# Performance work log

Hardware: AMD Instinct MI355X
Metric: run time of the kernel (lower is better)

The kernel has to match this reference:

```python
import jax, jax.numpy as jnp
import numpy as np

N_L = 1600   # sample_number_l
N_R = 64     # sample_number_r
F = 512      # num_rgbxyz_feature


def setup_inputs() -> dict:
    key = jax.random.key(0)
    ks = jax.random.split(key, 6)
    soutput_l = jax.random.normal(ks[0], (200000, F), dtype=jnp.float32)
    soutput_r = jax.random.normal(ks[1], (100000, F), dtype=jnp.float32)
    W1 = jax.random.normal(ks[2], (2 * F, 512), dtype=jnp.float32) * 0.02
    b1 = jnp.zeros((512,), dtype=jnp.float32)
    W2 = jax.random.normal(ks[3], (512, 2), dtype=jnp.float32) * 0.02
    b2 = jnp.zeros((2,), dtype=jnp.float32)
    sample_idx_l = jax.random.randint(ks[4], (N_L,), 0, 200000)
    sample_idx_r = jax.random.randint(ks[5], (N_R,), 0, 100000)
    return {
        'soutput_l': soutput_l, 'soutput_r': soutput_r,
        'W1': W1, 'b1': b1, 'W2': W2, 'b2': b2,
        'sample_idx_l': sample_idx_l, 'sample_idx_r': sample_idx_r,
    }


def reference(soutput_l, soutput_r, W1, b1, W2, b2, sample_idx_l, sample_idx_r):
    # Gather sampled per-point features (replaces torch.randint sampling)
    fl = soutput_l[sample_idx_l]          # [N_l, F]
    fr = soutput_r[sample_idx_r]          # [N_r, F]
    n_l, feat = fl.shape
    n_r = fr.shape[0]
    # All-pairs concat: equivalent to the python loop over the 64 right samples,
    # each doing cat((feat_l, feat_r[i].repeat(N_l,1)), dim=1)
    cat = jnp.concatenate([
        jnp.broadcast_to(fl[:, None, :], (n_l, n_r, feat)),
        jnp.broadcast_to(fr[None, :, :], (n_l, n_r, feat)),
    ], axis=-1)                            # [N_l, N_r, 2F]
    # base3DPoseNet: 2-layer MLP (no batch norm), logits over 2 classes
    h = jax.nn.relu(jnp.einsum('lrf,fh->lrh', cat, W1) + b1)   # [N_l, N_r, 512]
    logits = jnp.einsum('lrh,hc->lrc', h, W2) + b2             # [N_l, N_r, 2]
    # softmax over class dim, take P(match) -> correspondence_map[N_l, N_r]
    correspondence_map = jax.nn.softmax(logits, axis=-1)[..., 1]
    return correspondence_map
```

## Files before the change

kernel.cpp:

```cpp
#include <hip/hip_runtime.h>
#include <math.h>

#define FDIM 512
#define NL 1600
#define NR 64
#define NM (NL + NR)

typedef __attribute__((ext_vector_type(8))) short short8;
typedef __attribute__((ext_vector_type(4))) float f32x4;
typedef __attribute__((ext_vector_type(8))) unsigned short ushort8;
typedef __attribute__((ext_vector_type(4))) unsigned short ushort4v;

__device__ __forceinline__ unsigned short f2bf(float f) {
    unsigned u = __float_as_uint(f);
    u += 0x7fffu + ((u >> 16) & 1u);
    return (unsigned short)(u >> 16);
}

__global__ __launch_bounds__(256) void k_prep(
    const float* __restrict__ SL, const float* __restrict__ SR,
    const float* __restrict__ W1, const float* __restrict__ W2,
    const int* __restrict__ idxL, const int* __restrict__ idxR,
    unsigned short* __restrict__ Abf, unsigned short* __restrict__ WT,
    float* __restrict__ wd)
{
    __shared__ float tile[32][33];
    const int t = threadIdx.x;
    if (blockIdx.x == 928) {
        float4 v = *(const float4*)(&W2[t * 4]);
        wd[2 * t]     = v.y - v.x;
        wd[2 * t + 1] = v.w - v.z;
        return;
    }
    if (blockIdx.x < 416) {
        const int rowi = blockIdx.x * 4 + (t >> 6);
        const int k0 = (t & 63) * 8;
        long srow; const float* sp;
        if (rowi < NL) { srow = idxL[rowi];      sp = SL; }
        else           { srow = idxR[rowi - NL]; sp = SR; }
        const float* p = sp + srow * FDIM + k0;
        float4 v0 = *(const float4*)(p);
        float4 v1 = *(const float4*)(p + 4);
        ushort8 o;
        o[0]=f2bf(v0.x); o[1]=f2bf(v0.y); o[2]=f2bf(v0.z); o[3]=f2bf(v0.w);
        o[4]=f2bf(v1.x); o[5]=f2bf(v1.y); o[6]=f2bf(v1.z); o[7]=f2bf(v1.w);
        *(ushort8*)(Abf + (long)rowi * FDIM + k0) = o;
    } else {
        const int bidx = blockIdx.x - 416;
        const int ktile = bidx >> 4;
        const int ntile = bidx & 15;
        {
            const int r  = t >> 3;
            const int c4 = (t & 7) * 4;
            float4 v = *(const float4*)(&W1[(long)(ktile*32 + r) * FDIM + ntile*32 + c4]);
            tile[r][c4+0]=v.x; tile[r][c4+1]=v.y; tile[r][c4+2]=v.z; tile[r][c4+3]=v.w;
        }
        __syncthreads();
        const int h  = ktile >> 4;
        const int kb = (ktile & 15) * 32;
        const int nl = t >> 3;
        const int k4 = (t & 7) * 4;
        ushort4v o;
        o[0]=f2bf(tile[k4+0][nl]); o[1]=f2bf(tile[k4+1][nl]);
        o[2]=f2bf(tile[k4+2][nl]); o[3]=f2bf(tile[k4+3][nl]);
        *(ushort4v*)(WT + (long)h*FDIM*FDIM + (long)(ntile*32 + nl)*FDIM + kb + k4) = o;
    }
}

__global__ __launch_bounds__(64) void k_mfma(
    const short* __restrict__ Abf, const short* __restrict__ WT,
    const float* __restrict__ b1, float* __restrict__ A, float* __restrict__ Bm)
{
    const int bm = blockIdx.x;
    const int bn = blockIdx.y;
    const bool isB = bm >= 50;
    const int m0 = bm * 32, n0 = bn * 64;
    const short* wt = WT + (isB ? (long)FDIM * FDIM : 0);
    const int lane = threadIdx.x;
    const int row = lane & 15, g = lane >> 4;

    f32x4 acc[2][4] = {};
    const short* aP = Abf + (long)(m0 + row) * FDIM + g * 8;
    const short* bP = wt  + (long)(n0 + row) * FDIM + g * 8;

    short8 a[6][2], b[6][4];
    #pragma unroll
    for (int s = 0; s < 6; ++s) {
        #pragma unroll
        for (int i = 0; i < 2; i++) a[s][i] = *(const short8*)(aP + s * 32 + i * 16 * FDIM);
        #pragma unroll
        for (int j = 0; j < 4; j++) b[s][j] = *(const short8*)(bP + s * 32 + j * 16 * FDIM);
    }

    #pragma unroll
    for (int kk = 0; kk < 16; ++kk) {
        const int cur = kk % 6;
        #pragma unroll
        for (int i = 0; i < 2; i++)
            #pragma unroll
            for (int j = 0; j < 4; j++)
                acc[i][j] = __builtin_amdgcn_mfma_f32_16x16x32_bf16(a[cur][i], b[cur][j], acc[i][j], 0, 0, 0);
        if (kk < 10) {
            const int ko = (kk + 6) * 32;
            #pragma unroll
            for (int i = 0; i < 2; i++) a[cur][i] = *(const short8*)(aP + ko + i * 16 * FDIM);
            #pragma unroll
            for (int j = 0; j < 4; j++) b[cur][j] = *(const short8*)(bP + ko + j * 16 * FDIM);
        }
    }

    #pragma unroll
    for (int i = 0; i < 2; i++) {
        #pragma unroll
        for (int j = 0; j < 4; j++) {
            #pragma unroll
            for (int r = 0; r < 4; r++) {
                const int m = m0 + i * 16 + g * 4 + r;
                const int n = n0 + j * 16 + row;
                const float v = acc[i][j][r];
                if (isB) Bm[(long)(m - NL) * FDIM + n] = v + b1[n];
                else     A [(long)m * FDIM + n] = v;
            }
        }
    }
}

__global__ __launch_bounds__(256) void k_pair(
    const float* __restrict__ A, const float* __restrict__ Bm,
    const float* __restrict__ wd, float* __restrict__ Part)
{
    __shared__ float4 Bs[16 * 64];
    const int t    = threadIdx.x;
    const int lane = t & 63;
    const int w    = t >> 6;
    const int lt   = blockIdx.x;
    const int kq   = blockIdx.y;

    const float4* Bm4 = (const float4*)Bm;
    #pragma unroll
    for (int i = 0; i < 4; ++i) {
        const int idx = i * 256 + t;
        const int r = idx >> 4, c = idx & 15;
        Bs[c * 64 + (r ^ c)] = Bm4[r * 128 + kq * 16 + c];
    }
    __syncthreads();

    const int lb = lt * 16 + w * 4;
    const float4* A0 = (const float4*)(A + (long)(lb + 0) * FDIM) + kq * 16;
    const float4* A1 = (const float4*)(A + (long)(lb + 1) * FDIM) + kq * 16;
    const float4* A2 = (const float4*)(A + (long)(lb + 2) * FDIM) + kq * 16;
    const float4* A3 = (const float4*)(A + (long)(lb + 3) * FDIM) + kq * 16;
    const float4* W4 = (const float4*)wd + kq * 16;

    float acc0 = 0.f, acc1 = 0.f, acc2 = 0.f, acc3 = 0.f;
    #pragma unroll
    for (int c = 0; c < 16; ++c) {
        float4 b  = Bs[c * 64 + (lane ^ c)];
        float4 wv = W4[c];
        float4 a0 = A0[c], a1 = A1[c], a2 = A2[c], a3 = A3[c];
        acc0 = fmaf(fmaxf(a0.x + b.x, 0.f), wv.x, acc0);
        acc0 = fmaf(fmaxf(a0.y + b.y, 0.f), wv.y, acc0);
        acc0 = fmaf(fmaxf(a0.z + b.z, 0.f), wv.z, acc0);
        acc0 = fmaf(fmaxf(a0.w + b.w, 0.f), wv.w, acc0);
        acc1 = fmaf(fmaxf(a1.x + b.x, 0.f), wv.x, acc1);
        acc1 = fmaf(fmaxf(a1.y + b.y, 0.f), wv.y, acc1);
        acc1 = fmaf(fmaxf(a1.z + b.z, 0.f), wv.z, acc1);
        acc1 = fmaf(fmaxf(a1.w + b.w, 0.f), wv.w, acc1);
        acc2 = fmaf(fmaxf(a2.x + b.x, 0.f), wv.x, acc2);
        acc2 = fmaf(fmaxf(a2.y + b.y, 0.f), wv.y, acc2);
        acc2 = fmaf(fmaxf(a2.z + b.z, 0.f), wv.z, acc2);
        acc2 = fmaf(fmaxf(a2.w + b.w, 0.f), wv.w, acc2);
        acc3 = fmaf(fmaxf(a3.x + b.x, 0.f), wv.x, acc3);
        acc3 = fmaf(fmaxf(a3.y + b.y, 0.f), wv.y, acc3);
        acc3 = fmaf(fmaxf(a3.z + b.z, 0.f), wv.z, acc3);
        acc3 = fmaf(fmaxf(a3.w + b.w, 0.f), wv.w, acc3);
    }
    float* P = Part + ((long)kq * NL + lb) * NR + lane;
    P[0 * NR] = acc0;
    P[1 * NR] = acc1;
    P[2 * NR] = acc2;
    P[3 * NR] = acc3;
}

__global__ __launch_bounds__(256) void k_final(
    const float* __restrict__ Part, const float* __restrict__ b2,
    float* __restrict__ out)
{
    const int gid = blockIdx.x * 256 + threadIdx.x;
    float s = b2[1] - b2[0];
    #pragma unroll
    for (int q = 0; q < 8; ++q) s += Part[(long)q * NL * NR + gid];
    out[gid] = 1.f / (1.f + expf(-s));
}

extern "C" void kernel_launch(void* const* d_in, const int* in_sizes, int n_in,
                              void* d_out, int out_size, void* d_ws, size_t ws_size,
                              hipStream_t stream) {
    const float* SL  = (const float*)d_in[0];
    const float* SR  = (const float*)d_in[1];
    const float* W1  = (const float*)d_in[2];
    const float* b1  = (const float*)d_in[3];
    const float* W2  = (const float*)d_in[4];
    const float* b2  = (const float*)d_in[5];
    const int*   idxL = (const int*)d_in[6];
    const int*   idxR = (const int*)d_in[7];
    float* out = (float*)d_out;

    float* A    = (float*)d_ws;
    float* Bm   = A + (long)NL * FDIM;
    float* wd   = Bm + (long)NR * FDIM;
    float* Part = wd + FDIM;
    unsigned short* Abf = (unsigned short*)(Part + (long)8 * NL * NR);
    unsigned short* WT  = Abf + (long)NM * FDIM;

    k_prep<<<929, 256, 0, stream>>>(SL, SR, W1, W2, idxL, idxR, Abf, WT, wd);
    k_mfma<<<dim3(52, 8), 64, 0, stream>>>((const short*)Abf, (const short*)WT, b1, A, Bm);
    k_pair<<<dim3(100, 8), 256, 0, stream>>>(A, Bm, wd, Part);
    k_final<<<(NL * NR) / 256, 256, 0, stream>>>(Part, b2, out);
}
```

Baseline: 35.32 us.

## Fuse gather and bf16 conversion into MFMA GEMM, drop prep kernel

Removes the separate prep kernel. The GEMM now gathers fp32 rows directly by index, reads W1 in its original layout with strided scalar loads, and converts to bf16 in registers using v_cvt_pk_bf16_f32. The GEMM tile shrinks to 32x32 with a 2-stage register pipeline, doubling the grid along N, and the W2 difference vector is now computed per block in k_pair's shared memory. This saves one launch and the bf16 workspace round trip. In exchange, W1 loads are uncoalesced column-strided reads and each block re-reads its gathered A rows.

```diff
diff --git a/kernel.cpp b/kernel.cpp
--- a/kernel.cpp
+++ b/kernel.cpp
@@ -4,138 +4,136 @@
 #define FDIM 512
 #define NL 1600
 #define NR 64
-#define NM (NL + NR)
 
 typedef __attribute__((ext_vector_type(8))) short short8;
 typedef __attribute__((ext_vector_type(4))) float f32x4;
-typedef __attribute__((ext_vector_type(8))) unsigned short ushort8;
-typedef __attribute__((ext_vector_type(4))) unsigned short ushort4v;
-
-__device__ __forceinline__ unsigned short f2bf(float f) {
-    unsigned u = __float_as_uint(f);
-    u += 0x7fffu + ((u >> 16) & 1u);
-    return (unsigned short)(u >> 16);
-}
-
-__global__ __launch_bounds__(256) void k_prep(
+typedef __attribute__((ext_vector_type(4))) int   int4v;
+
+__device__ __forceinline__ int cvtpk(float lo, float hi) {
+    int r;
+    asm("v_cvt_pk_bf16_f32 %0, %1, %2" : "=v"(r) : "v"(lo), "v"(hi));
+    return r;
+}
+
+__global__ __launch_bounds__(64) void k_gemm(
     const float* __restrict__ SL, const float* __restrict__ SR,
-    const float* __restrict__ W1, const float* __restrict__ W2,
+    const float* __restrict__ W1, const float* __restrict__ b1,
     const int* __restrict__ idxL, const int* __restrict__ idxR,
-    unsigned short* __restrict__ Abf, unsigned short* __restrict__ WT,
-    float* __restrict__ wd)
-{
-    __shared__ float tile[32][33];
-    const int t = threadIdx.x;
-    if (blockIdx.x == 928) {
-        float4 v = *(const float4*)(&W2[t * 4]);
-        wd[2 * t]     = v.y - v.x;
-        wd[2 * t + 1] = v.w - v.z;
-        return;
-    }
-    if (blockIdx.x < 416) {
-        const int rowi = blockIdx.x * 4 + (t >> 6);
-        const int k0 = (t & 63) * 8;
-        long srow; const float* sp;
-        if (rowi < NL) { srow = idxL[rowi];      sp = SL; }
-        else           { srow = idxR[rowi - NL]; sp = SR; }
-        const float* p = sp + srow * FDIM + k0;
-        float4 v0 = *(const float4*)(p);
-        float4 v1 = *(const float4*)(p + 4);
-        ushort8 o;
-        o[0]=f2bf(v0.x); o[1]=f2bf(v0.y); o[2]=f2bf(v0.z); o[3]=f2bf(v0.w);
-        o[4]=f2bf(v1.x); o[5]=f2bf(v1.y); o[6]=f2bf(v1.z); o[7]=f2bf(v1.w);
-        *(ushort8*)(Abf + (long)rowi * FDIM + k0) = o;
-    } else {
-        const int bidx = blockIdx.x - 416;
-        const int ktile = bidx >> 4;
-        const int ntile = bidx & 15;
-        {
-            const int r  = t >> 3;
-            const int c4 = (t & 7) * 4;
-            float4 v = *(const float4*)(&W1[(long)(ktile*32 + r) * FDIM + ntile*32 + c4]);
-            tile[r][c4+0]=v.x; tile[r][c4+1]=v.y; tile[r][c4+2]=v.z; tile[r][c4+3]=v.w;
-        }
-        __syncthreads();
-        const int h  = ktile >> 4;
-        const int kb = (ktile & 15) * 32;
-        const int nl = t >> 3;
-        const int k4 = (t & 7) * 4;
-        ushort4v o;
-        o[0]=f2bf(tile[k4+0][nl]); o[1]=f2bf(tile[k4+1][nl]);
-        o[2]=f2bf(tile[k4+2][nl]); o[3]=f2bf(tile[k4+3][nl]);
-        *(ushort4v*)(WT + (long)h*FDIM*FDIM + (long)(ntile*32 + nl)*FDIM + kb + k4) = o;
-    }
-}
-
-__global__ __launch_bounds__(64) void k_mfma(
-    const short* __restrict__ Abf, const short* __restrict__ WT,
-    const float* __restrict__ b1, float* __restrict__ A, float* __restrict__ Bm)
+    float* __restrict__ A, float* __restrict__ Bm)
 {
     const int bm = blockIdx.x;
     const int bn = blockIdx.y;
     const bool isB = bm >= 50;
-    const int m0 = bm * 32, n0 = bn * 64;
-    const short* wt = WT + (isB ? (long)FDIM * FDIM : 0);
-    const int lane = threadIdx.x;
-    const int row = lane & 15, g = lane >> 4;
-
-    f32x4 acc[2][4] = {};
-    const short* aP = Abf + (long)(m0 + row) * FDIM + g * 8;
-    const short* bP = wt  + (long)(n0 + row) * FDIM + g * 8;
-
-    short8 a[6][2], b[6][4];
-    #pragma unroll
-    for (int s = 0; s < 6; ++s) {
+    const int n0 = bn * 32;
+    const int lane = threadIdx.x, row = lane & 15, g = lane >> 4;
+
+    const float* a0p; const float* a1p;
+    if (isB) {
+        const int rb = (bm - 50) * 32;
+        a0p = SR + (long)idxR[rb + row] * FDIM;
+        a1p = SR + (long)idxR[rb + 16 + row] * FDIM;
+    } else {
+        const int mb = bm * 32;
+        a0p = SL + (long)idxL[mb + row] * FDIM;
+        a1p = SL + (long)idxL[mb + 16 + row] * FDIM;
+    }
+    const float* w0 = W1 + (isB ? (long)FDIM * FDIM : 0) + (n0 + row);
+    const float* w1 = w0 + 16;
+
+    f32x4 acc00 = {}, acc01 = {}, acc10 = {}, acc11 = {};
+    float4 a0r[2][2], a1r[2][2];
+    float  b0r[2][8], b1r[2][8];
+
+    {
+        a0r[0][0] = *(const float4*)(a0p + g * 8);
+        a0r[0][1] = *(const float4*)(a0p + g * 8 + 4);
+        a1r[0][0] = *(const float4*)(a1p + g * 8);
+        a1r[0][1] = *(const float4*)(a1p + g * 8 + 4);
         #pragma unroll
-        for (int i = 0; i < 2; i++) a[s][i] = *(const short8*)(aP + s * 32 + i * 16 * FDIM);
-        #pragma unroll
-        for (int j = 0; j < 4; j++) b[s][j] = *(const short8*)(bP + s * 32 + j * 16 * FDIM);
+        for (int jj = 0; jj < 8; ++jj) {
+            b0r[0][jj] = w0[(long)(g * 8 + jj) * FDIM];
+            b1r[0][jj] = w1[(long)(g * 8 + jj) * FDIM];
+        }
     }
 
     #pragma unroll
     for (int kk = 0; kk < 16; ++kk) {
-        const int cur = kk % 6;
-        #pragma unroll
-        for (int i = 0; i < 2; i++)
+        const int cur = kk & 1, nxt = cur ^ 1;
+        if (kk < 15) {
+            const int kb = (kk + 1) * 32 + g * 8;
+            a0r[nxt][0] = *(const float4*)(a0p + kb);
+            a0r[nxt][1] = *(const float4*)(a0p + kb + 4);
+            a1r[nxt][0] = *(const float4*)(a1p + kb);
+            a1r[nxt][1] = *(const float4*)(a1p + kb + 4);
             #pragma unroll
-            for (int j = 0; j < 4; j++)
-                acc[i][j] = __builtin_amdgcn_mfma_f32_16x16x32_bf16(a[cur][i], b[cur][j], acc[i][j], 0, 0, 0);
-        if (kk < 10) {
-            const int ko = (kk + 6) * 32;
-            #pragma unroll
-            for (int i = 0; i < 2; i++) a[cur][i] = *(const short8*)(aP + ko + i * 16 * FDIM);
-            #pragma unroll
-            for (int j = 0; j < 4; j++) b[cur][j] = *(const short8*)(bP + ko + j * 16 * FDIM);
-        }
-    }
-
-    #pragma unroll
-    for (int i = 0; i < 2; i++) {
-        #pragma unroll
-        for (int j = 0; j < 4; j++) {
-            #pragma unroll
-            for (int r = 0; r < 4; r++) {
-                const int m = m0 + i * 16 + g * 4 + r;
-                const int n = n0 + j * 16 + row;
-                const float v = acc[i][j][r];
-                if (isB) Bm[(long)(m - NL) * FDIM + n] = v + b1[n];
-                else     A [(long)m * FDIM + n] = v;
+            for (int jj = 0; jj < 8; ++jj) {
+                b0r[nxt][jj] = w0[(long)(kb + jj) * FDIM];
+                b1r[nxt][jj] = w1[(long)(kb + jj) * FDIM];
             }
         }
+        int4v a0, a1, b0, b1;
+        a0.x = cvtpk(a0r[cur][0].x, a0r[cur][0].y);
+        a0.y = cvtpk(a0r[cur][0].z, a0r[cur][0].w);
+        a0.z = cvtpk(a0r[cur][1].x, a0r[cur][1].y);
+        a0.w = cvtpk(a0r[cur][1].z, a0r[cur][1].w);
+        a1.x = cvtpk(a1r[cur][0].x, a1r[cur][0].y);
+        a1.y = cvtpk(a1r[cur][0].z, a1r[cur][0].w);
+        a1.z = cvtpk(a1r[cur][1].x, a1r[cur][1].y);
+        a1.w = cvtpk(a1r[cur][1].z, a1r[cur][1].w);
+        b0.x = cvtpk(b0r[cur][0], b0r[cur][1]);
+        b0.y = cvtpk(b0r[cur][2], b0r[cur][3]);
+        b0.z = cvtpk(b0r[cur][4], b0r[cur][5]);
+        b0.w = cvtpk(b0r[cur][6], b0r[cur][7]);
+        b1.x = cvtpk(b1r[cur][0], b1r[cur][1]);
+        b1.y = cvtpk(b1r[cur][2], b1r[cur][3]);
+        b1.z = cvtpk(b1r[cur][4], b1r[cur][5]);
+        b1.w = cvtpk(b1r[cur][6], b1r[cur][7]);
+        const short8 A0 = *(const short8*)&a0, A1 = *(const short8*)&a1;
+        const short8 B0 = *(const short8*)&b0, B1 = *(const short8*)&b1;
+        acc00 = __builtin_amdgcn_mfma_f32_16x16x32_bf16(A0, B0, acc00, 0, 0, 0);
+        acc01 = __builtin_amdgcn_mfma_f32_16x16x32_bf16(A0, B1, acc01, 0, 0, 0);
+        acc10 = __builtin_amdgcn_mfma_f32_16x16x32_bf16(A1, B0, acc10, 0, 0, 0);
+        acc11 = __builtin_amdgcn_mfma_f32_16x16x32_bf16(A1, B1, acc11, 0, 0, 0);
+    }
+
+    #pragma unroll
+    for (int r = 0; r < 4; ++r) {
+        const int na = n0 + row, nb = n0 + 16 + row;
+        const int mr0 = g * 4 + r, mr1 = 16 + g * 4 + r;
+        if (isB) {
+            const int rb = (bm - 50) * 32;
+            const float ba = b1[na], bb = b1[nb];
+            Bm[(long)(rb + mr0) * FDIM + na] = acc00[r] + ba;
+            Bm[(long)(rb + mr0) * FDIM + nb] = acc01[r] + bb;
+            Bm[(long)(rb + mr1) * FDIM + na] = acc10[r] + ba;
+            Bm[(long)(rb + mr1) * FDIM + nb] = acc11[r] + bb;
+        } else {
+            const int mb = bm * 32;
+            A[(long)(mb + mr0) * FDIM + na] = acc00[r];
+            A[(long)(mb + mr0) * FDIM + nb] = acc01[r];
+            A[(long)(mb + mr1) * FDIM + na] = acc10[r];
+            A[(long)(mb + mr1) * FDIM + nb] = acc11[r];
+        }
     }
 }
 
 __global__ __launch_bounds__(256) void k_pair(
     const float* __restrict__ A, const float* __restrict__ Bm,
-    const float* __restrict__ wd, float* __restrict__ Part)
+    const float* __restrict__ W2, float* __restrict__ Part)
 {
     __shared__ float4 Bs[16 * 64];
+    __shared__ float wdl[64];
     const int t    = threadIdx.x;
     const int lane = t & 63;
     const int w    = t >> 6;
     const int lt   = blockIdx.x;
     const int kq   = blockIdx.y;
 
+    if (t < 32) {
+        float4 v = *(const float4*)(&W2[kq * 128 + 4 * t]);
+        wdl[2 * t]     = v.y - v.x;
+        wdl[2 * t + 1] = v.w - v.z;
+    }
     const float4* Bm4 = (const float4*)Bm;
     #pragma unroll
     for (int i = 0; i < 4; ++i) {
@@ -150,7 +148,7 @@
     const float4* A1 = (const float4*)(A + (long)(lb + 1) * FDIM) + kq * 16;
     const float4* A2 = (const float4*)(A + (long)(lb + 2) * FDIM) + kq * 16;
     const float4* A3 = (const float4*)(A + (long)(lb + 3) * FDIM) + kq * 16;
-    const float4* W4 = (const float4*)wd + kq * 16;
+    const float4* W4 = (const float4*)wdl;
 
     float acc0 = 0.f, acc1 = 0.f, acc2 = 0.f, acc3 = 0.f;
     #pragma unroll
@@ -208,13 +206,9 @@
 
     float* A    = (float*)d_ws;
     float* Bm   = A + (long)NL * FDIM;
-    float* wd   = Bm + (long)NR * FDIM;
-    float* Part = wd + FDIM;
-    unsigned short* Abf = (unsigned short*)(Part + (long)8 * NL * NR);
-    unsigned short* WT  = Abf + (long)NM * FDIM;
-
-    k_prep<<<929, 256, 0, stream>>>(SL, SR, W1, W2, idxL, idxR, Abf, WT, wd);
-    k_mfma<<<dim3(52, 8), 64, 0, stream>>>((const short*)Abf, (const short*)WT, b1, A, Bm);
-    k_pair<<<dim3(100, 8), 256, 0, stream>>>(A, Bm, wd, Part);
+    float* Part = Bm + (long)NR * FDIM;
+
+    k_gemm<<<dim3(52, 16), 64, 0, stream>>>(SL, SR, W1, b1, idxL, idxR, A, Bm);
+    k_pair<<<dim3(100, 8), 256, 0, stream>>>(A, Bm, W2, Part);
     k_final<<<(NL * NR) / 256, 256, 0, stream>>>(Part, b2, out);
 }
```

After: 30.01 us. 1.18x faster.
